# Kernel tuning notes

Measured on AMD Instinct MI355X. Metric: run time of the kernel, lower is better.

The kernel has to match this reference:

```python
import jax, jax.numpy as jnp
import numpy as np

EPS = 1e-5  # torch InstanceNorm2d / LayerNorm default eps


def setup_inputs() -> dict:
    key = jax.random.key(0)
    k1, k2, k3 = jax.random.split(key, 3)
    B, C, H, W_ = 8, 256, 128, 128
    x = jax.random.normal(k1, (B, C, H, W_), dtype=jnp.float32)
    params = jax.random.normal(k2, (B, 2 * C), dtype=jnp.float32)
    # Conv2d(dim*2, dim, 1) weight, squeezed to [C_out, C_in]
    W = jax.random.normal(k3, (C, 2 * C), dtype=jnp.float32) * (1.0 / np.sqrt(2 * C))
    return {"x": x, "params": params, "W": W}


def reference(x, params, W):
    # x: [B, C, H, W]; params: [B, 2C]; W: [C, 2C]
    C = x.shape[1]
    # InstanceNorm2d (no affine): normalize over spatial dims per (b, c), biased var
    in_mean = jnp.mean(x, axis=(2, 3), keepdims=True)
    in_var = jnp.var(x, axis=(2, 3), keepdims=True)
    IN = (x - in_mean) * jax.lax.rsqrt(in_var + EPS)
    # LayerNorm over (C, H, W) per sample, biased var
    ln_mean = jnp.mean(x, axis=(1, 2, 3), keepdims=True)
    ln_var = jnp.var(x, axis=(1, 2, 3), keepdims=True)
    LN = (x - ln_mean) * jax.lax.rsqrt(ln_var + EPS)
    LIN = jnp.concatenate((IN, LN), axis=1)  # [B, 2C, H, W]
    # 1x1 conv == channel contraction
    c = jnp.einsum('bihw,oi->bohw', LIN, W)  # [B, C, H, W]
    gamma = params[:, :C][:, :, None, None]
    beta = params[:, C:][:, :, None, None]
    return gamma * c + beta
```

## Files before the change

kernel.cpp:

```cpp
#include <hip/hip_runtime.h>
#include <stdint.h>

#define HW_  16384
#define CH   256
#define NB   8
#define EPSV 1e-5f

typedef float f32x4 __attribute__((ext_vector_type(4)));
typedef short s16x8 __attribute__((ext_vector_type(8)));

__device__ __forceinline__ unsigned short f2bf(float f) {
    union { float f; uint32_t u; } v; v.f = f;
    uint32_t r = (v.u + 0x7FFFu + ((v.u >> 16) & 1u)) >> 16;
    return (unsigned short)r;
}

__device__ __forceinline__ void glds16(const unsigned short* g, unsigned short* l) {
    __builtin_amdgcn_global_load_lds(
        (const __attribute__((address_space(1))) uint32_t*)g,
        (__attribute__((address_space(3))) uint32_t*)l,
        16, 0, 0);
}

__global__ __launch_bounds__(256) void stats_kernel(const float* __restrict__ x,
                                                    float* __restrict__ sums,
                                                    float* __restrict__ sumsq) {
    const int bc  = blockIdx.x;
    const int tid = threadIdx.x;
    const float4* p = reinterpret_cast<const float4*>(x + (size_t)bc * HW_);
    float s = 0.f, q = 0.f;
#pragma unroll 4
    for (int i = tid; i < HW_ / 4; i += 256) {
        float4 v = p[i];
        s += v.x + v.y + v.z + v.w;
        q += v.x * v.x + v.y * v.y + v.z * v.z + v.w * v.w;
    }
    __shared__ float rs[256], rq[256];
    rs[tid] = s; rq[tid] = q;
    __syncthreads();
    for (int off = 128; off > 0; off >>= 1) {
        if (tid < off) { rs[tid] += rs[tid + off]; rq[tid] += rq[tid + off]; }
        __syncthreads();
    }
    if (tid == 0) { sums[bc] = rs[0]; sumsq[bc] = rq[0]; }
}

__global__ __launch_bounds__(256) void prep_kernel(const float* __restrict__ sums,
                                                   const float* __restrict__ sumsq,
                                                   const float* __restrict__ params,
                                                   const float* __restrict__ W,
                                                   unsigned short* __restrict__ Ap,
                                                   float* __restrict__ Dp) {
    const int b   = blockIdx.x;
    const int tid = threadIdx.x;
    __shared__ float mu[CH], ri[CH], rs[CH], rq[CH];
    float s = sums[b * CH + tid];
    float q = sumsq[b * CH + tid];
    float m = s * (1.0f / HW_);
    float v = q * (1.0f / HW_) - m * m;
    mu[tid] = m;
    ri[tid] = rsqrtf(v + EPSV);
    rs[tid] = s; rq[tid] = q;
    __syncthreads();
    for (int off = 128; off > 0; off >>= 1) {
        if (tid < off) { rs[tid] += rs[tid + off]; rq[tid] += rq[tid + off]; }
        __syncthreads();
    }
    const float invN = 1.0f / ((float)CH * (float)HW_);
    const float mln  = rs[0] * invN;
    const float vln  = rq[0] * invN - mln * mln;
    const float rln  = rsqrtf(vln + EPSV);

    const int o = tid;
    const float gamma = params[b * 2 * CH + o];
    const float beta  = params[b * 2 * CH + CH + o];
    const float4* w1p = reinterpret_cast<const float4*>(W + (size_t)o * 2 * CH);
    const float4* w2p = reinterpret_cast<const float4*>(W + (size_t)o * 2 * CH + CH);
    unsigned short* aprow = Ap + ((size_t)(b * CH + o)) * CH;
    float t1 = 0.f, t2 = 0.f;
    for (int c4 = 0; c4 < CH / 4; ++c4) {
        float4 w1 = w1p[c4];
        float4 w2 = w2p[c4];
        float w1a[4] = {w1.x, w1.y, w1.z, w1.w};
        float w2a[4] = {w2.x, w2.y, w2.z, w2.w};
        const int c = c4 * 4;
        ushort4 pk;
        unsigned short* pka = (unsigned short*)&pk;
#pragma unroll
        for (int j = 0; j < 4; ++j) {
            float ric = ri[c + j];
            float a   = gamma * (w1a[j] * ric + w2a[j] * rln);
            pka[j] = f2bf(a);
            t1 += w1a[j] * ric * mu[c + j];
            t2 += w2a[j];
        }
        *reinterpret_cast<ushort4*>(aprow + c) = pk;
    }
    const float d = -(t1 + rln * mln * t2);
    Dp[b * CH + o] = gamma * d + beta;
}

__global__ __launch_bounds__(512, 4) void gemm_kernel(const float* __restrict__ x,
                                                      const unsigned short* __restrict__ Ap,
                                                      const float* __restrict__ Dp,
                                                      float* __restrict__ out) {
    __shared__ unsigned short As[2][4 * 256 * 8];
    __shared__ unsigned short Xs[2][4 * 128 * 8];

    const int b   = blockIdx.y;
    const int n0  = blockIdx.x * 128;
    const int t   = threadIdx.x;
    const int w   = t >> 6;
    const int l   = t & 63;
    const int wm  = w >> 1;
    const int wn  = w & 1;
    const int lhi = l >> 4;
    const int llo = l & 15;

    f32x4 acc[4][4];
    const float* dpb = Dp + b * CH;
#pragma unroll
    for (int fm = 0; fm < 4; ++fm) {
        f32x4 d = *reinterpret_cast<const f32x4*>(dpb + wm * 64 + fm * 16 + lhi * 4);
#pragma unroll
        for (int fn = 0; fn < 4; ++fn) acc[fm][fn] = d;
    }

    const size_t xbase = (size_t)b * CH * HW_ + n0;
    const unsigned short* apb = Ap + (size_t)b * CH * CH;
    uint32_t* Xs32 = reinterpret_cast<uint32_t*>(&Xs[0][0]);

    const int i0 = 2 * w,      i1 = 2 * w + 1;
    const int g0 = i0 & 3,     q0 = i0 >> 2;
    const int g1 = i1 & 3,     q1 = i1 >> 2;
    const unsigned short* aglob0 = apb + (size_t)(q0 * 64 + l) * CH + g0 * 8;
    const unsigned short* aglob1 = apb + (size_t)(q1 * 64 + l) * CH + g1 * 8;
    unsigned short* alds0 = &As[0][g0 * 2048 + q0 * 512];
    unsigned short* alds1 = &As[0][g1 * 2048 + q1 * 512];

    const int kp = t >> 5;
    const int nq = t & 31;
    const int xg = kp >> 2;
    const int xh = kp & 3;
    const float* xlane = x + xbase + (size_t)(2 * kp) * HW_ + nq * 4;

    int npr[4];
#pragma unroll
    for (int fn = 0; fn < 4; ++fn) {
        const int nr = wn * 64 + fn * 16 + llo;
        npr[fn] = nr ^ ((nr >> 3) & 7);
    }

    glds16(aglob0, alds0);
    glds16(aglob1, alds1);
    f32x4 xa[2], xb[2];
    xa[0] = *reinterpret_cast<const f32x4*>(xlane);
    xb[0] = *reinterpret_cast<const f32x4*>(xlane + HW_);
    xa[1] = *reinterpret_cast<const f32x4*>(xlane + (size_t)32 * HW_);
    xb[1] = *reinterpret_cast<const f32x4*>(xlane + (size_t)32 * HW_ + HW_);
#pragma unroll
    for (int j = 0; j < 4; ++j) {
        const int n  = nq * 4 + j;
        const int np = n ^ ((n >> 3) & 7);
        Xs32[xg * 512 + np * 4 + xh] =
            (uint32_t)f2bf(xa[0][j]) | ((uint32_t)f2bf(xb[0][j]) << 16);
    }

#pragma unroll
    for (int kb = 0; kb < 8; ++kb) {
        __syncthreads();
        const int cur = kb & 1, nxt = cur ^ 1;

        if (kb < 7) {
#pragma unroll
            for (int j = 0; j < 4; ++j) {
                const int n  = nq * 4 + j;
                const int np = n ^ ((n >> 3) & 7);
                Xs32[nxt * 2048 + xg * 512 + np * 4 + xh] =
                    (uint32_t)f2bf(xa[nxt][j]) | ((uint32_t)f2bf(xb[nxt][j]) << 16);
            }
            glds16(aglob0 + (kb + 1) * 32, alds0 + nxt * 8192);
            glds16(aglob1 + (kb + 1) * 32, alds1 + nxt * 8192);
        }
        if (kb < 6) {
            const float* xp = xlane + (size_t)(kb + 2) * 32 * HW_;
            xa[cur] = *reinterpret_cast<const f32x4*>(xp);
            xb[cur] = *reinterpret_cast<const f32x4*>(xp + HW_);
        }

        s16x8 af[4];
#pragma unroll
        for (int fm = 0; fm < 4; ++fm)
            af[fm] = *reinterpret_cast<const s16x8*>(&As[cur][lhi * 2048 + (wm * 64 + fm * 16 + llo) * 8]);
#pragma unroll
        for (int fn = 0; fn < 4; ++fn) {
            s16x8 bfr = *reinterpret_cast<const s16x8*>(&Xs[cur][lhi * 1024 + npr[fn] * 8]);
#pragma unroll
            for (int fm = 0; fm < 4; ++fm)
                acc[fm][fn] = __builtin_amdgcn_mfma_f32_16x16x32_bf16(af[fm], bfr, acc[fm][fn], 0, 0, 0);
        }
    }

#pragma unroll
    for (int fm = 0; fm < 4; ++fm) {
        const int m = wm * 64 + fm * 16 + lhi * 4;
        float* obase = out + (size_t)(b * CH + m) * HW_ + n0 + wn * 64 + llo;
#pragma unroll
        for (int fn = 0; fn < 4; ++fn) {
#pragma unroll
            for (int r = 0; r < 4; ++r)
                obase[(size_t)r * HW_ + fn * 16] = acc[fm][fn][r];
        }
    }
}

extern "C" void kernel_launch(void* const* d_in, const int* in_sizes, int n_in,
                              void* d_out, int out_size, void* d_ws, size_t ws_size,
                              hipStream_t stream) {
    const float* x      = (const float*)d_in[0];
    const float* params = (const float*)d_in[1];
    const float* W      = (const float*)d_in[2];
    float* out = (float*)d_out;
    float* ws  = (float*)d_ws;

    float* sums  = ws;
    float* sumsq = ws + 2048;
    float* Dp    = ws + 4096;
    unsigned short* Ap = (unsigned short*)(ws + 6144);

    hipLaunchKernelGGL(stats_kernel, dim3(NB * CH), dim3(256), 0, stream, x, sums, sumsq);
    hipLaunchKernelGGL(prep_kernel,  dim3(NB),      dim3(256), 0, stream, sums, sumsq, params, W, Ap, Dp);
    hipLaunchKernelGGL(gemm_kernel,  dim3(HW_ / 128, NB), dim3(512), 0, stream, x, Ap, Dp, out);
}
```

Baseline: 112.9 us.

## Fuse stats with bf16 transpose of x and feed GEMM via direct LDS loads

The statistics kernel now also converts x to bf16 in a GEMM-ready transposed tile layout in workspace, and writes per-tile partial sums that prep reduces. The GEMM streams this pre-packed tile straight into LDS with global_load_lds instead of loading fp32 x, converting it and storing it to LDS itself. This removes conversion and register staging from the GEMM loop but adds a bf16 intermediate write and read. It also drops the LDS swizzle on the B tile, which may cause bank conflicts.

```diff
diff --git a/kernel.cpp b/kernel.cpp
--- a/kernel.cpp
+++ b/kernel.cpp
@@ -4,6 +4,7 @@
 #define HW_  16384
 #define CH   256
 #define NB   8
+#define NT   128
 #define EPSV 1e-5f
 
 typedef float f32x4 __attribute__((ext_vector_type(4)));
@@ -22,31 +23,71 @@
         16, 0, 0);
 }
 
-__global__ __launch_bounds__(256) void stats_kernel(const float* __restrict__ x,
-                                                    float* __restrict__ sums,
-                                                    float* __restrict__ sumsq) {
-    const int bc  = blockIdx.x;
-    const int tid = threadIdx.x;
-    const float4* p = reinterpret_cast<const float4*>(x + (size_t)bc * HW_);
-    float s = 0.f, q = 0.f;
+__global__ __launch_bounds__(256) void tstat_kernel(const float* __restrict__ x,
+                                                    unsigned short* __restrict__ xT,
+                                                    float* __restrict__ partS,
+                                                    float* __restrict__ partQ) {
+    const int b  = blockIdx.y;
+    const int bx = blockIdx.x;
+    const int n0 = bx * 128;
+    const int t  = threadIdx.x;
+
+    __shared__ uint32_t T2[128 * 132];
+
+    const float* xb = x + (size_t)b * CH * HW_ + n0;
+
 #pragma unroll 4
-    for (int i = tid; i < HW_ / 4; i += 256) {
-        float4 v = p[i];
-        s += v.x + v.y + v.z + v.w;
-        q += v.x * v.x + v.y * v.y + v.z * v.z + v.w * v.w;
-    }
-    __shared__ float rs[256], rq[256];
-    rs[tid] = s; rq[tid] = q;
+    for (int it = 0; it < 16; ++it) {
+        const int cp = it * 8 + (t >> 5);
+        const int n4 = (t & 31) * 4;
+        const float* pa = xb + (size_t)(2 * cp) * HW_ + n4;
+        f32x4 va = *reinterpret_cast<const f32x4*>(pa);
+        f32x4 vb = *reinterpret_cast<const f32x4*>(pa + HW_);
+
+        float sA = va[0] + va[1] + va[2] + va[3];
+        float qA = va[0]*va[0] + va[1]*va[1] + va[2]*va[2] + va[3]*va[3];
+        float sB = vb[0] + vb[1] + vb[2] + vb[3];
+        float qB = vb[0]*vb[0] + vb[1]*vb[1] + vb[2]*vb[2] + vb[3]*vb[3];
+#pragma unroll
+        for (int off = 1; off < 32; off <<= 1) {
+            sA += __shfl_xor(sA, off, 32);
+            qA += __shfl_xor(qA, off, 32);
+            sB += __shfl_xor(sB, off, 32);
+            qB += __shfl_xor(qB, off, 32);
+        }
+        if ((t & 31) == 0) {
+            partS[(size_t)(b * CH + 2 * cp    ) * NT + bx] = sA;
+            partQ[(size_t)(b * CH + 2 * cp    ) * NT + bx] = qA;
+            partS[(size_t)(b * CH + 2 * cp + 1) * NT + bx] = sB;
+            partQ[(size_t)(b * CH + 2 * cp + 1) * NT + bx] = qB;
+        }
+
+        uint4 pk;
+        pk.x = (uint32_t)f2bf(va[0]) | ((uint32_t)f2bf(vb[0]) << 16);
+        pk.y = (uint32_t)f2bf(va[1]) | ((uint32_t)f2bf(vb[1]) << 16);
+        pk.z = (uint32_t)f2bf(va[2]) | ((uint32_t)f2bf(vb[2]) << 16);
+        pk.w = (uint32_t)f2bf(va[3]) | ((uint32_t)f2bf(vb[3]) << 16);
+        *reinterpret_cast<uint4*>(&T2[cp * 132 + n4]) = pk;
+    }
     __syncthreads();
-    for (int off = 128; off > 0; off >>= 1) {
-        if (tid < off) { rs[tid] += rs[tid + off]; rq[tid] += rq[tid + off]; }
-        __syncthreads();
-    }
-    if (tid == 0) { sums[bc] = rs[0]; sumsq[bc] = rq[0]; }
-}
-
-__global__ __launch_bounds__(256) void prep_kernel(const float* __restrict__ sums,
-                                                   const float* __restrict__ sumsq,
+
+    uint4* dst = reinterpret_cast<uint4*>(xT + ((size_t)(b * NT + bx)) * (128 * CH));
+#pragma unroll 4
+    for (int it = 0; it < 16; ++it) {
+        const int idx = it * 256 + t;
+        const int g   = idx >> 7;
+        const int n   = idx & 127;
+        uint4 o;
+        o.x = T2[(g * 4 + 0) * 132 + n];
+        o.y = T2[(g * 4 + 1) * 132 + n];
+        o.z = T2[(g * 4 + 2) * 132 + n];
+        o.w = T2[(g * 4 + 3) * 132 + n];
+        dst[idx] = o;
+    }
+}
+
+__global__ __launch_bounds__(256) void prep_kernel(const float* __restrict__ partS,
+                                                   const float* __restrict__ partQ,
                                                    const float* __restrict__ params,
                                                    const float* __restrict__ W,
                                                    unsigned short* __restrict__ Ap,
@@ -54,8 +95,17 @@
     const int b   = blockIdx.x;
     const int tid = threadIdx.x;
     __shared__ float mu[CH], ri[CH], rs[CH], rq[CH];
-    float s = sums[b * CH + tid];
-    float q = sumsq[b * CH + tid];
+
+    float s = 0.f, q = 0.f;
+    const f32x4* ps = reinterpret_cast<const f32x4*>(partS + (size_t)(b * CH + tid) * NT);
+    const f32x4* pq = reinterpret_cast<const f32x4*>(partQ + (size_t)(b * CH + tid) * NT);
+#pragma unroll 8
+    for (int i = 0; i < NT / 4; ++i) {
+        f32x4 a = ps[i], c4 = pq[i];
+        s += a[0] + a[1] + a[2] + a[3];
+        q += c4[0] + c4[1] + c4[2] + c4[3];
+    }
+
     float m = s * (1.0f / HW_);
     float v = q * (1.0f / HW_) - m * m;
     mu[tid] = m;
@@ -78,12 +128,12 @@
     const float4* w2p = reinterpret_cast<const float4*>(W + (size_t)o * 2 * CH + CH);
     unsigned short* aprow = Ap + ((size_t)(b * CH + o)) * CH;
     float t1 = 0.f, t2 = 0.f;
-    for (int c4 = 0; c4 < CH / 4; ++c4) {
-        float4 w1 = w1p[c4];
-        float4 w2 = w2p[c4];
+    for (int c4i = 0; c4i < CH / 4; ++c4i) {
+        float4 w1 = w1p[c4i];
+        float4 w2 = w2p[c4i];
         float w1a[4] = {w1.x, w1.y, w1.z, w1.w};
         float w2a[4] = {w2.x, w2.y, w2.z, w2.w};
-        const int c = c4 * 4;
+        const int c = c4i * 4;
         ushort4 pk;
         unsigned short* pka = (unsigned short*)&pk;
 #pragma unroll
@@ -100,7 +150,7 @@
     Dp[b * CH + o] = gamma * d + beta;
 }
 
-__global__ __launch_bounds__(512, 4) void gemm_kernel(const float* __restrict__ x,
+__global__ __launch_bounds__(512, 4) void gemm_kernel(const unsigned short* __restrict__ xT,
                                                       const unsigned short* __restrict__ Ap,
                                                       const float* __restrict__ Dp,
                                                       float* __restrict__ out) {
@@ -108,7 +158,8 @@
     __shared__ unsigned short Xs[2][4 * 128 * 8];
 
     const int b   = blockIdx.y;
-    const int n0  = blockIdx.x * 128;
+    const int bx  = blockIdx.x;
+    const int n0  = bx * 128;
     const int t   = threadIdx.x;
     const int w   = t >> 6;
     const int l   = t & 63;
@@ -126,9 +177,8 @@
         for (int fn = 0; fn < 4; ++fn) acc[fm][fn] = d;
     }
 
-    const size_t xbase = (size_t)b * CH * HW_ + n0;
     const unsigned short* apb = Ap + (size_t)b * CH * CH;
-    uint32_t* Xs32 = reinterpret_cast<uint32_t*>(&Xs[0][0]);
+    const unsigned short* xtb = xT + ((size_t)(b * NT + bx)) * (128 * CH);
 
     const int i0 = 2 * w,      i1 = 2 * w + 1;
     const int g0 = i0 & 3,     q0 = i0 >> 2;
@@ -138,33 +188,13 @@
     unsigned short* alds0 = &As[0][g0 * 2048 + q0 * 512];
     unsigned short* alds1 = &As[0][g1 * 2048 + q1 * 512];
 
-    const int kp = t >> 5;
-    const int nq = t & 31;
-    const int xg = kp >> 2;
-    const int xh = kp & 3;
-    const float* xlane = x + xbase + (size_t)(2 * kp) * HW_ + nq * 4;
-
-    int npr[4];
-#pragma unroll
-    for (int fn = 0; fn < 4; ++fn) {
-        const int nr = wn * 64 + fn * 16 + llo;
-        npr[fn] = nr ^ ((nr >> 3) & 7);
-    }
+    const int gl = w >> 1, nh = w & 1;
+    const unsigned short* xglob = xtb + (size_t)((gl * 128) + nh * 64 + l) * 8;
+    unsigned short* xlds = &Xs[0][(gl * 128 + nh * 64) * 8];
 
     glds16(aglob0, alds0);
     glds16(aglob1, alds1);
-    f32x4 xa[2], xb[2];
-    xa[0] = *reinterpret_cast<const f32x4*>(xlane);
-    xb[0] = *reinterpret_cast<const f32x4*>(xlane + HW_);
-    xa[1] = *reinterpret_cast<const f32x4*>(xlane + (size_t)32 * HW_);
-    xb[1] = *reinterpret_cast<const f32x4*>(xlane + (size_t)32 * HW_ + HW_);
-#pragma unroll
-    for (int j = 0; j < 4; ++j) {
-        const int n  = nq * 4 + j;
-        const int np = n ^ ((n >> 3) & 7);
-        Xs32[xg * 512 + np * 4 + xh] =
-            (uint32_t)f2bf(xa[0][j]) | ((uint32_t)f2bf(xb[0][j]) << 16);
-    }
+    glds16(xglob,  xlds);
 
 #pragma unroll
     for (int kb = 0; kb < 8; ++kb) {
@@ -172,20 +202,9 @@
         const int cur = kb & 1, nxt = cur ^ 1;
 
         if (kb < 7) {
-#pragma unroll
-            for (int j = 0; j < 4; ++j) {
-                const int n  = nq * 4 + j;
-                const int np = n ^ ((n >> 3) & 7);
-                Xs32[nxt * 2048 + xg * 512 + np * 4 + xh] =
-                    (uint32_t)f2bf(xa[nxt][j]) | ((uint32_t)f2bf(xb[nxt][j]) << 16);
-            }
-            glds16(aglob0 + (kb + 1) * 32, alds0 + nxt * 8192);
-            glds16(aglob1 + (kb + 1) * 32, alds1 + nxt * 8192);
-        }
-        if (kb < 6) {
-            const float* xp = xlane + (size_t)(kb + 2) * 32 * HW_;
-            xa[cur] = *reinterpret_cast<const f32x4*>(xp);
-            xb[cur] = *reinterpret_cast<const f32x4*>(xp + HW_);
+            glds16(aglob0 + (kb + 1) * 32,   alds0 + nxt * 8192);
+            glds16(aglob1 + (kb + 1) * 32,   alds1 + nxt * 8192);
+            glds16(xglob  + (kb + 1) * 4096, xlds  + nxt * 4096);
         }
 
         s16x8 af[4];
@@ -194,7 +213,8 @@
             af[fm] = *reinterpret_cast<const s16x8*>(&As[cur][lhi * 2048 + (wm * 64 + fm * 16 + llo) * 8]);
 #pragma unroll
         for (int fn = 0; fn < 4; ++fn) {
-            s16x8 bfr = *reinterpret_cast<const s16x8*>(&Xs[cur][lhi * 1024 + npr[fn] * 8]);
+            const int nr = wn * 64 + fn * 16 + llo;
+            s16x8 bfr = *reinterpret_cast<const s16x8*>(&Xs[cur][lhi * 1024 + nr * 8]);
 #pragma unroll
             for (int fm = 0; fm < 4; ++fm)
                 acc[fm][fn] = __builtin_amdgcn_mfma_f32_16x16x32_bf16(af[fm], bfr, acc[fm][fn], 0, 0, 0);
@@ -221,14 +241,15 @@
     const float* params = (const float*)d_in[1];
     const float* W      = (const float*)d_in[2];
     float* out = (float*)d_out;
-    float* ws  = (float*)d_ws;
-
-    float* sums  = ws;
-    float* sumsq = ws + 2048;
-    float* Dp    = ws + 4096;
-    unsigned short* Ap = (unsigned short*)(ws + 6144);
-
-    hipLaunchKernelGGL(stats_kernel, dim3(NB * CH), dim3(256), 0, stream, x, sums, sumsq);
-    hipLaunchKernelGGL(prep_kernel,  dim3(NB),      dim3(256), 0, stream, sums, sumsq, params, W, Ap, Dp);
-    hipLaunchKernelGGL(gemm_kernel,  dim3(HW_ / 128, NB), dim3(512), 0, stream, x, Ap, Dp, out);
-}
+    char*  ws  = (char*)d_ws;
+
+    float*          partS = (float*)(ws + 0);
+    float*          partQ = (float*)(ws + (1u << 20));
+    float*          Dp    = (float*)(ws + (2u << 20));
+    unsigned short* Ap    = (unsigned short*)(ws + (3u << 20));
+    unsigned short* xT    = (unsigned short*)(ws + (4u << 20));
+
+    hipLaunchKernelGGL(tstat_kernel, dim3(NT, NB), dim3(256), 0, stream, x, xT, partS, partQ);
+    hipLaunchKernelGGL(prep_kernel,  dim3(NB),     dim3(256), 0, stream, partS, partQ, params, W, Ap, Dp);
+    hipLaunchKernelGGL(gemm_kernel,  dim3(NT, NB), dim3(512), 0, stream, xT, Ap, Dp, out);
+}
```

New measurement: 156.9 us. +38.9%, slower.
